# Kernel tuning notes

Measured on AMD Instinct MI355X. Metric: run time of the kernel, lower is better.

Reference implementation:

```python
import jax, jax.numpy as jnp
import numpy as np

N_IN, N_OUT, N_HID, N_RES = 16, 2, 256, 256
B, L = 64, 2048
ALPHA_FAST, ALPHA_SLOW, SIGMA_NEU = 1.0, 0.1, 0.05


def _linear_params(k, n_out, n_in):
    # mimics torch nn.Linear default init: U(-1/sqrt(fan_in), 1/sqrt(fan_in))
    bound = 1.0 / np.sqrt(n_in)
    kw, kb = jax.random.split(k)
    W = jax.random.uniform(kw, (n_out, n_in), minval=-bound, maxval=bound, dtype=jnp.float32)
    b = jax.random.uniform(kb, (n_out,), minval=-bound, maxval=bound, dtype=jnp.float32)
    return W, b


def setup_inputs() -> dict:
    key = jax.random.key(0)
    ks = jax.random.split(key, 11)
    W_in, b_in = _linear_params(ks[0], N_HID, N_IN)
    W_hh, b_hh = _linear_params(ks[1], N_HID, N_HID)
    W_sf, b_sf = _linear_params(ks[2], N_HID, N_RES)
    W_fs, b_fs = _linear_params(ks[3], N_RES, N_HID)
    W_res, b_res = _linear_params(ks[4], N_RES, N_RES)
    W_out, b_out = _linear_params(ks[5], N_OUT, N_HID)
    W_pr, b_pr = _linear_params(ks[6], N_IN, N_RES)
    input_signal = jax.random.normal(ks[7], (B, L, N_IN), dtype=jnp.float32)
    hidden = jax.random.normal(ks[8], (B, N_HID), dtype=jnp.float32)
    reservoir = jax.random.normal(ks[9], (B, N_RES), dtype=jnp.float32)
    # neural noise: randn * sigma_neu * sqrt(alpha_fast), precomputed time-major [L,B,H]
    noise = jax.random.normal(ks[10], (L, B, N_HID), dtype=jnp.float32) * (SIGMA_NEU * np.sqrt(ALPHA_FAST))
    return dict(input_signal=input_signal, hidden=hidden, reservoir=reservoir, noise=noise,
                W_in=W_in, b_in=b_in, W_hh=W_hh, b_hh=b_hh, W_sf=W_sf, b_sf=b_sf,
                W_fs=W_fs, b_fs=b_fs, W_res=W_res, b_res=b_res,
                W_out=W_out, b_out=b_out, W_pr=W_pr, b_pr=b_pr, length=L)


def reference(input_signal, hidden, reservoir, noise,
              W_in, b_in, W_hh, b_hh, W_sf, b_sf, W_fs, b_fs,
              W_res, b_res, W_out, b_out, W_pr, b_pr, length):
    xs = jnp.transpose(input_signal, (1, 0, 2))  # [L, B, n_in], time-major like torch permute
    af = jnp.float32(ALPHA_FAST)
    asl = jnp.float32(ALPHA_SLOW)

    def step(carry, inp):
        h, r = carry
        x_t, nz = inp
        tmp_h = jax.nn.relu(x_t @ W_in.T + b_in + h @ W_hh.T + b_hh + r @ W_sf.T + b_sf)
        tmp_r = jax.nn.relu(h @ W_fs.T + b_fs + r @ W_res.T + b_res)
        h = (1.0 - af) * h + af * tmp_h + nz
        r = (1.0 - asl) * r + asl * tmp_r
        out = jnp.clip(h @ W_out.T + b_out, -2.0, 2.0)
        prior = jax.nn.sigmoid(r @ W_pr.T + b_pr)
        return (h, r), (h, out, prior)

    _, (hs, outs, priors) = jax.lax.scan(step, (hidden, reservoir), (xs, noise))
    # back to batch-major [B, L, .]
    return (jnp.transpose(hs, (1, 0, 2)),
            jnp.transpose(outs, (1, 0, 2)),
            jnp.transpose(priors, (1, 0, 2)))
```

## Files before the change

kernel.cpp:

```cpp
#include <hip/hip_runtime.h>
#include <stdint.h>
#include <stddef.h>

#define LT    2048
#define BATCH 64
#define NH    256
#define HS_ELEMS  (BATCH * LT * NH)
#define OUT_ELEMS (BATCH * LT * 2)

typedef __attribute__((ext_vector_type(8))) __bf16 bf16x8;
typedef __attribute__((ext_vector_type(4))) float  f32x4;
typedef __attribute__((ext_vector_type(2))) unsigned u32x2;
typedef __attribute__((ext_vector_type(8))) unsigned short u16x8;

static __device__ __forceinline__ unsigned pk2(float a, float b) {
  unsigned r;
  asm("v_cvt_pk_bf16_f32 %0, %1, %2" : "=v"(r) : "v"(a), "v"(b));
  return r;
}
static __device__ __forceinline__ bf16x8 pack8v(f32x4 a, f32x4 b) {
  union { unsigned u[4]; bf16x8 v; } r;
  r.u[0] = pk2(a[0], a[1]); r.u[1] = pk2(a[2], a[3]);
  r.u[2] = pk2(b[0], b[1]); r.u[3] = pk2(b[2], b[3]);
  return r.v;
}
static __device__ __forceinline__ bf16x8 pack8(const float* p) {
  return pack8v(*(const f32x4*)p, *(const f32x4*)(p + 4));
}
static __device__ __forceinline__ float bf2f(unsigned short u) {
  unsigned v = ((unsigned)u) << 16;
  return __builtin_bit_cast(float, v);
}

#define BARRIER() do {                                           \
    asm volatile("s_waitcnt lgkmcnt(0)" ::: "memory");           \
    __builtin_amdgcn_s_barrier();                                \
    asm volatile("" ::: "memory");                               \
  } while (0)

#define W_RES_OFF 0
#define A_S0_OFF  131072
#define A_S1_OFF  147456
#define LDS_BYTES 163840

__global__ __launch_bounds__(256) void u_precompute_kernel(
    const float* __restrict__ x,
    const float* __restrict__ W_in,
    const float* __restrict__ b_in,
    const float* __restrict__ b_hh,
    const float* __restrict__ b_sf,
    float* __restrict__ u)
{
  __shared__ float xs[64][16];
  const int tid = threadIdx.x;
  const int b  = blockIdx.x >> 5;
  const int tc = (blockIdx.x & 31) << 6;
  float w[16];
#pragma unroll
  for (int i = 0; i < 16; ++i) w[i] = W_in[tid * 16 + i];
  const float bias = b_in[tid] + b_hh[tid] + b_sf[tid];
  for (int r = tid; r < 64 * 16; r += 256)
    xs[r >> 4][r & 15] = x[((size_t)b * LT + tc + (r >> 4)) * 16 + (r & 15)];
  __syncthreads();
  for (int tt = 0; tt < 64; ++tt) {
    float s = bias;
#pragma unroll
    for (int i = 0; i < 16; ++i) s += xs[tt][i] * w[i];
    u[((size_t)b * LT + tc + tt) * NH + tid] = s;
  }
}

template<int PRIOR_MODE>
__global__ __launch_bounds__(512, 1) void rnn_seq_kernel(
    const float* __restrict__ hidden,
    const float* __restrict__ reservoir,
    const float* __restrict__ noise,
    const float* __restrict__ W_hh, const float* __restrict__ W_sf,
    const float* __restrict__ W_fs, const float* __restrict__ W_res,
    const float* __restrict__ b_fs, const float* __restrict__ b_res,
    const float* __restrict__ W_pr, const float* __restrict__ b_pr,
    float* __restrict__ hs,
    float* __restrict__ priors,
    unsigned short* __restrict__ rws)
{
  extern __shared__ char lds[];
  const int tid  = threadIdx.x;
  const int lane = tid & 63;
  const int wv   = tid >> 6;
  const int col  = lane & 15;
  const int kg   = lane >> 4;
  const int b0   = blockIdx.x * 16;

#pragma unroll 4
  for (int j = 0; j < 16; ++j) {
    const int c   = j * 512 + tid;
    const int kk8 = c >> 10, n = (c >> 2) & 255, kgs = c & 3;
    *(bf16x8*)(lds + W_RES_OFF + c * 16) =
        pack8(W_res + (size_t)n * NH + kk8 * 32 + kgs * 8);
  }
  {
    const int kk = tid >> 6, l16 = tid & 63;
    const int kgs = l16 >> 4, m = l16 & 15;
    *(bf16x8*)(lds + A_S0_OFF + tid * 16) =
        pack8(hidden + (size_t)(b0 + m) * NH + kk * 32 + kgs * 8);
    *(bf16x8*)(lds + A_S0_OFF + (tid + 512) * 16) =
        pack8(reservoir + (size_t)(b0 + m) * NH + kk * 32 + kgs * 8);
  }

  bf16x8 wHH[2][8], wSF[2][8], wFS[2][8];
  f32x4 biasrR[2];
#pragma unroll
  for (int tile = 0; tile < 2; ++tile) {
    const int n = wv * 32 + tile * 16 + col;
#pragma unroll
    for (int kk = 0; kk < 8; ++kk) {
      wHH[tile][kk] = pack8(W_hh + (size_t)n * NH + kk * 32 + kg * 8);
      wSF[tile][kk] = pack8(W_sf + (size_t)n * NH + kk * 32 + kg * 8);
      wFS[tile][kk] = pack8(W_fs + (size_t)n * NH + kk * 32 + kg * 8);
    }
    const int nb = wv * 32 + tile * 16 + kg * 4;
    f32x4 bf = *(const f32x4*)(b_fs + nb);
    f32x4 br = *(const f32x4*)(b_res + nb);
    biasrR[tile] = bf + br;
  }
  bf16x8 wPR[PRIOR_MODE ? 8 : 1];
  f32x4 bp4;
  if (PRIOR_MODE) {
#pragma unroll
    for (int kk8 = 0; kk8 < 8; ++kk8)
      wPR[kk8] = pack8(W_pr + (size_t)col * NH + kk8 * 32 + kg * 8);
    bp4 = *(const f32x4*)(b_pr + kg * 4);
  }

  const size_t hsRow = (size_t)(b0 + col) * (LT * NH);
  const size_t nzRow = (size_t)(b0 + col) * NH;
  f32x4 r_old[2], accH[2], accR[2], accP;
#pragma unroll
  for (int tile = 0; tile < 2; ++tile) {
    const int nb = wv * 32 + tile * 16 + kg * 4;
    r_old[tile] = *(const f32x4*)(reservoir + nzRow + nb);
    accH[tile]  = *(const f32x4*)(hs + hsRow + nb);
    accR[tile]  = biasrR[tile];
  }
  if (PRIOR_MODE) accP = bp4;

  BARRIER();

#pragma unroll 1
  for (int t = 0; t < LT; ++t) {
    const size_t tp1 = (t + 1 < LT) ? (size_t)(t + 1) : (size_t)(LT - 1);
    f32x4 pfU[2], nzc[2];
#pragma unroll
    for (int tile = 0; tile < 2; ++tile) {
      const int nb = wv * 32 + tile * 16 + kg * 4;
      pfU[tile] = *(const f32x4*)(hs + hsRow + tp1 * NH + nb);
      nzc[tile] = *(const f32x4*)(noise + (size_t)t * (BATCH * NH) + nzRow + nb);
    }

    const char* afp = lds + A_S0_OFF + (t & 1) * 16384 + lane * 16;
    const char* bwp = lds + W_RES_OFF + (wv * 32) * 64 + col * 64 + kg * 16;
#pragma unroll
    for (int kk = 0; kk < 16; ++kk) {
      const bf16x8 af = *(const bf16x8*)(afp + kk * 1024);
      if (kk < 8) {
#pragma unroll
        for (int tile = 0; tile < 2; ++tile)
          accH[tile] = __builtin_amdgcn_mfma_f32_16x16x32_bf16(wHH[tile][kk], af, accH[tile], 0, 0, 0);
#pragma unroll
        for (int tile = 0; tile < 2; ++tile)
          accR[tile] = __builtin_amdgcn_mfma_f32_16x16x32_bf16(wFS[tile][kk], af, accR[tile], 0, 0, 0);
      } else {
#pragma unroll
        for (int tile = 0; tile < 2; ++tile)
          accH[tile] = __builtin_amdgcn_mfma_f32_16x16x32_bf16(wSF[tile][kk - 8], af, accH[tile], 0, 0, 0);
#pragma unroll
        for (int tile = 0; tile < 2; ++tile) {
          const bf16x8 bw = *(const bf16x8*)(bwp + (kk - 8) * 16384 + tile * 1024);
          accR[tile] = __builtin_amdgcn_mfma_f32_16x16x32_bf16(bw, af, accR[tile], 0, 0, 0);
        }
        if (PRIOR_MODE && wv == 1) {
          accP = __builtin_amdgcn_mfma_f32_16x16x32_bf16(wPR[kk - 8], af, accP, 0, 0, 0);
        }
      }
    }

    float* hsT = hs + hsRow + (size_t)t * NH;
    unsigned short* wsT = rws + ((size_t)(b0 + col) * LT + (size_t)t) * NH;
    char* abase = lds + A_S0_OFF + ((t + 1) & 1) * 16384 +
                  wv * 1024 + col * 16 + (kg & 1) * 8;
#pragma unroll
    for (int tile = 0; tile < 2; ++tile) {
      const int nb = wv * 32 + tile * 16 + kg * 4;
      f32x4 hv, rv;
#pragma unroll
      for (int j = 0; j < 4; ++j) {
        hv[j] = fmaxf(accH[tile][j], 0.f) + nzc[tile][j];
        rv[j] = 0.9f * r_old[tile][j] + 0.1f * fmaxf(accR[tile][j], 0.f);
      }
      r_old[tile] = rv;
      *(f32x4*)(hsT + nb) = hv;
      u32x2 hp, rp;
      hp[0] = pk2(hv[0], hv[1]); hp[1] = pk2(hv[2], hv[3]);
      rp[0] = pk2(rv[0], rv[1]); rp[1] = pk2(rv[2], rv[3]);
      char* dst = abase + (2 * tile + (kg >> 1)) * 256;
      *(u32x2*)dst          = hp;
      *(u32x2*)(dst + 8192) = rp;
      if (!PRIOR_MODE)
        *(u32x2*)(wsT + nb) = rp;
    }
    if (PRIOR_MODE && wv == 1 && t > 0) {
      f32x4 pv;
#pragma unroll
      for (int j = 0; j < 4; ++j) pv[j] = 1.f / (1.f + __expf(-accP[j]));
      *(f32x4*)(priors + (size_t)(b0 + col) * (LT * 16) + (size_t)(t - 1) * 16 + kg * 4) = pv;
    }

#pragma unroll
    for (int tile = 0; tile < 2; ++tile) {
      accH[tile] = pfU[tile];
      accR[tile] = biasrR[tile];
    }
    if (PRIOR_MODE) accP = bp4;
    BARRIER();
  }

  if (PRIOR_MODE && wv == 1) {
    f32x4 aP = bp4;
    const char* afp2 = lds + A_S0_OFF + 8192 + lane * 16;
#pragma unroll
    for (int kk8 = 0; kk8 < 8; ++kk8) {
      const bf16x8 af = *(const bf16x8*)(afp2 + kk8 * 1024);
      aP = __builtin_amdgcn_mfma_f32_16x16x32_bf16(wPR[kk8], af, aP, 0, 0, 0);
    }
    f32x4 pv;
#pragma unroll
    for (int j = 0; j < 4; ++j) pv[j] = 1.f / (1.f + __expf(-aP[j]));
    *(f32x4*)(priors + (size_t)(b0 + col) * (LT * 16) + (size_t)(LT - 1) * 16 + kg * 4) = pv;
  }
}

__global__ __launch_bounds__(256) void prior_post_kernel(
    const unsigned short* __restrict__ rws,
    const float* __restrict__ W_pr,
    const float* __restrict__ b_pr,
    float* __restrict__ priors)
{
  __shared__ unsigned short rs[64 * 256];
  const int tid = threadIdx.x;
  const int b  = blockIdx.x >> 5;
  const int tc = (blockIdx.x & 31) << 6;
  const unsigned short* src = rws + ((size_t)b * LT + tc) * NH;
  for (int i = tid; i < 2048; i += 256)
    *(((u16x8*)rs) + i) = *(((const u16x8*)src) + i);
  __syncthreads();
  const int n = tid & 15, tg = tid >> 4;
  const float* wrow = W_pr + n * NH;
  const float bp = b_pr[n];
  float s0 = bp, s1 = bp, s2 = bp, s3 = bp;
  const unsigned short* r0 = rs + (tg * 4 + 0) * NH;
#pragma unroll 8
  for (int k8 = 0; k8 < 32; ++k8) {
    const f32x4 w0 = *(const f32x4*)(wrow + k8 * 8);
    const f32x4 w1 = *(const f32x4*)(wrow + k8 * 8 + 4);
    const u16x8 a = *(const u16x8*)(r0 + k8 * 8);
    const u16x8 bq = *(const u16x8*)(r0 + NH + k8 * 8);
    const u16x8 c = *(const u16x8*)(r0 + 2 * NH + k8 * 8);
    const u16x8 d = *(const u16x8*)(r0 + 3 * NH + k8 * 8);
#pragma unroll
    for (int j = 0; j < 4; ++j) {
      s0 += bf2f(a[j]) * w0[j] + bf2f(a[j + 4]) * w1[j];
      s1 += bf2f(bq[j]) * w0[j] + bf2f(bq[j + 4]) * w1[j];
      s2 += bf2f(c[j]) * w0[j] + bf2f(c[j + 4]) * w1[j];
      s3 += bf2f(d[j]) * w0[j] + bf2f(d[j + 4]) * w1[j];
    }
  }
  float* dst = priors + ((size_t)b * LT + tc + tg * 4) * 16 + n;
  dst[0]  = 1.f / (1.f + __expf(-s0));
  dst[16] = 1.f / (1.f + __expf(-s1));
  dst[32] = 1.f / (1.f + __expf(-s2));
  dst[48] = 1.f / (1.f + __expf(-s3));
}

__global__ __launch_bounds__(256) void out_project_kernel(
    const float* __restrict__ hs,
    const float* __restrict__ W_out,
    const float* __restrict__ b_out,
    float* __restrict__ outs)
{
  const int tid = threadIdx.x;
  const int lane = tid & 63;
  const int wv = tid >> 6;
  const int row0 = blockIdx.x * 64 + wv * 16;
  f32x4 w0 = *(const f32x4*)(W_out + lane * 4);
  f32x4 w1 = *(const f32x4*)(W_out + 256 + lane * 4);
  const float bo0 = b_out[0], bo1 = b_out[1];
  for (int i = 0; i < 16; ++i) {
    const f32x4 h = *(const f32x4*)(hs + (size_t)(row0 + i) * NH + lane * 4);
    float p0 = h[0]*w0[0] + h[1]*w0[1] + h[2]*w0[2] + h[3]*w0[3];
    float p1 = h[0]*w1[0] + h[1]*w1[1] + h[2]*w1[2] + h[3]*w1[3];
#pragma unroll
    for (int off = 32; off; off >>= 1) {
      p0 += __shfl_down(p0, off, 64);
      p1 += __shfl_down(p1, off, 64);
    }
    if (lane == 0) {
      const size_t o = (size_t)(row0 + i) * 2;
      outs[o]     = fminf(fmaxf(p0 + bo0, -2.f), 2.f);
      outs[o + 1] = fminf(fmaxf(p1 + bo1, -2.f), 2.f);
    }
  }
}

extern "C" void kernel_launch(void* const* d_in, const int* in_sizes, int n_in,
                              void* d_out, int out_size, void* d_ws, size_t ws_size,
                              hipStream_t stream) {
  const float* x         = (const float*)d_in[0];
  const float* hidden    = (const float*)d_in[1];
  const float* reservoir = (const float*)d_in[2];
  const float* noise     = (const float*)d_in[3];
  const float* W_in      = (const float*)d_in[4];
  const float* b_in      = (const float*)d_in[5];
  const float* W_hh      = (const float*)d_in[6];
  const float* b_hh      = (const float*)d_in[7];
  const float* W_sf      = (const float*)d_in[8];
  const float* b_sf      = (const float*)d_in[9];
  const float* W_fs      = (const float*)d_in[10];
  const float* b_fs      = (const float*)d_in[11];
  const float* W_res     = (const float*)d_in[12];
  const float* b_res     = (const float*)d_in[13];
  const float* W_out     = (const float*)d_in[14];
  const float* b_out     = (const float*)d_in[15];
  const float* W_pr      = (const float*)d_in[16];
  const float* b_pr      = (const float*)d_in[17];

  float* hs     = (float*)d_out;
  float* outs   = hs + HS_ELEMS;
  float* priors = outs + OUT_ELEMS;
  unsigned short* rws = (unsigned short*)d_ws;

  const size_t rws_bytes = (size_t)BATCH * LT * NH * sizeof(unsigned short);

  u_precompute_kernel<<<2048, 256, 0, stream>>>(x, W_in, b_in, b_hh, b_sf, hs);

  if (ws_size >= rws_bytes) {
    hipFuncSetAttribute((const void*)&rnn_seq_kernel<0>,
                        hipFuncAttributeMaxDynamicSharedMemorySize, LDS_BYTES);
    rnn_seq_kernel<0><<<4, 512, LDS_BYTES, stream>>>(
        hidden, reservoir, noise, W_hh, W_sf, W_fs, W_res,
        b_fs, b_res, W_pr, b_pr, hs, priors, rws);
    prior_post_kernel<<<2048, 256, 0, stream>>>(rws, W_pr, b_pr, priors);
  } else {
    hipFuncSetAttribute((const void*)&rnn_seq_kernel<1>,
                        hipFuncAttributeMaxDynamicSharedMemorySize, LDS_BYTES);
    rnn_seq_kernel<1><<<4, 512, LDS_BYTES, stream>>>(
        hidden, reservoir, noise, W_hh, W_sf, W_fs, W_res,
        b_fs, b_res, W_pr, b_pr, hs, priors, rws);
  }

  out_project_kernel<<<2048, 256, 0, stream>>>(hs, W_out, b_out, outs);
}
```

Baseline: 6.530 ms.

## Halve recurrent kernel to 4 waves with single-buffered LDS state and coalesced reservoir spill

The sequential RNN kernel now runs 256 threads (4 waves) per block instead of 512, so each wave handles 64 output columns (4 tiles) and keeps three times as many weight fragments in registers. The double-buffered activation area is replaced by a single buffer with an extra barrier between the MFMA reads and the state writeback, and the combined reservoir bias moves into LDS. The bf16 reservoir spill is written in a thread-contiguous layout that the prior post-kernel unscatters through LDS. Fewer waves per barrier should cut synchronisation cost on this latency-bound recurrence, but each wave does twice the serial MFMA work per step, register pressure grows sharply, and the PRIOR_MODE path still gates on wv==1 with the old column mapping, so that fallback may be inconsistent.

Measured after the change: 9.099 ms. 1.39x slower.

```diff
diff --git a/kernel.cpp b/kernel.cpp
--- a/kernel.cpp
+++ b/kernel.cpp
@@ -39,9 +39,9 @@
   } while (0)
 
 #define W_RES_OFF 0
-#define A_S0_OFF  131072
-#define A_S1_OFF  147456
-#define LDS_BYTES 163840
+#define A_S_OFF   131072
+#define BIASR_OFF 147456
+#define LDS_BYTES 148480
 
 __global__ __launch_bounds__(256) void u_precompute_kernel(
     const float* __restrict__ x,
@@ -71,7 +71,7 @@
 }
 
 template<int PRIOR_MODE>
-__global__ __launch_bounds__(512, 1) void rnn_seq_kernel(
+__global__ __launch_bounds__(256, 1) void rnn_seq_kernel(
     const float* __restrict__ hidden,
     const float* __restrict__ reservoir,
     const float* __restrict__ noise,
@@ -81,7 +81,7 @@
     const float* __restrict__ W_pr, const float* __restrict__ b_pr,
     float* __restrict__ hs,
     float* __restrict__ priors,
-    unsigned short* __restrict__ rws)
+    u32x2* __restrict__ rws8)
 {
   extern __shared__ char lds[];
   const int tid  = threadIdx.x;
@@ -92,36 +92,38 @@
   const int b0   = blockIdx.x * 16;
 
 #pragma unroll 4
-  for (int j = 0; j < 16; ++j) {
-    const int c   = j * 512 + tid;
+  for (int j = 0; j < 32; ++j) {
+    const int c   = j * 256 + tid;
     const int kk8 = c >> 10, n = (c >> 2) & 255, kgs = c & 3;
     *(bf16x8*)(lds + W_RES_OFF + c * 16) =
         pack8(W_res + (size_t)n * NH + kk8 * 32 + kgs * 8);
   }
-  {
-    const int kk = tid >> 6, l16 = tid & 63;
+#pragma unroll
+  for (int half = 0; half < 2; ++half) {
+    const int c = half * 256 + tid;
+    const int kk = c >> 6, l16 = c & 63;
     const int kgs = l16 >> 4, m = l16 & 15;
-    *(bf16x8*)(lds + A_S0_OFF + tid * 16) =
+    *(bf16x8*)(lds + A_S_OFF + c * 16) =
         pack8(hidden + (size_t)(b0 + m) * NH + kk * 32 + kgs * 8);
-    *(bf16x8*)(lds + A_S0_OFF + (tid + 512) * 16) =
+    *(bf16x8*)(lds + A_S_OFF + (c + 512) * 16) =
         pack8(reservoir + (size_t)(b0 + m) * NH + kk * 32 + kgs * 8);
   }
-
-  bf16x8 wHH[2][8], wSF[2][8], wFS[2][8];
-  f32x4 biasrR[2];
-#pragma unroll
-  for (int tile = 0; tile < 2; ++tile) {
-    const int n = wv * 32 + tile * 16 + col;
+  if (tid < 64) {
+    f32x4 v = *(const f32x4*)(b_fs + tid * 4);
+    f32x4 w = *(const f32x4*)(b_res + tid * 4);
+    *(f32x4*)(lds + BIASR_OFF + tid * 16) = v + w;
+  }
+
+  bf16x8 wHH[4][8], wSF[4][8], wFS[4][8];
+#pragma unroll
+  for (int tile = 0; tile < 4; ++tile) {
+    const int n = wv * 64 + tile * 16 + col;
 #pragma unroll
     for (int kk = 0; kk < 8; ++kk) {
       wHH[tile][kk] = pack8(W_hh + (size_t)n * NH + kk * 32 + kg * 8);
       wSF[tile][kk] = pack8(W_sf + (size_t)n * NH + kk * 32 + kg * 8);
       wFS[tile][kk] = pack8(W_fs + (size_t)n * NH + kk * 32 + kg * 8);
     }
-    const int nb = wv * 32 + tile * 16 + kg * 4;
-    f32x4 bf = *(const f32x4*)(b_fs + nb);
-    f32x4 br = *(const f32x4*)(b_res + nb);
-    biasrR[tile] = bf + br;
   }
   bf16x8 wPR[PRIOR_MODE ? 8 : 1];
   f32x4 bp4;
@@ -134,13 +136,13 @@
 
   const size_t hsRow = (size_t)(b0 + col) * (LT * NH);
   const size_t nzRow = (size_t)(b0 + col) * NH;
-  f32x4 r_old[2], accH[2], accR[2], accP;
-#pragma unroll
-  for (int tile = 0; tile < 2; ++tile) {
-    const int nb = wv * 32 + tile * 16 + kg * 4;
+  f32x4 r_old[4], accH[4], accR[4], accP;
+#pragma unroll
+  for (int tile = 0; tile < 4; ++tile) {
+    const int nb = wv * 64 + tile * 16 + kg * 4;
     r_old[tile] = *(const f32x4*)(reservoir + nzRow + nb);
     accH[tile]  = *(const f32x4*)(hs + hsRow + nb);
-    accR[tile]  = biasrR[tile];
+    accR[tile]  = *(const f32x4*)(lds + BIASR_OFF + nb * 4);
   }
   if (PRIOR_MODE) accP = bp4;
 
@@ -149,32 +151,32 @@
 #pragma unroll 1
   for (int t = 0; t < LT; ++t) {
     const size_t tp1 = (t + 1 < LT) ? (size_t)(t + 1) : (size_t)(LT - 1);
-    f32x4 pfU[2], nzc[2];
-#pragma unroll
-    for (int tile = 0; tile < 2; ++tile) {
-      const int nb = wv * 32 + tile * 16 + kg * 4;
+    f32x4 pfU[4], nzc[4];
+#pragma unroll
+    for (int tile = 0; tile < 4; ++tile) {
+      const int nb = wv * 64 + tile * 16 + kg * 4;
       pfU[tile] = *(const f32x4*)(hs + hsRow + tp1 * NH + nb);
       nzc[tile] = *(const f32x4*)(noise + (size_t)t * (BATCH * NH) + nzRow + nb);
     }
 
-    const char* afp = lds + A_S0_OFF + (t & 1) * 16384 + lane * 16;
-    const char* bwp = lds + W_RES_OFF + (wv * 32) * 64 + col * 64 + kg * 16;
+    const char* afp = lds + A_S_OFF + lane * 16;
+    const char* bwp = lds + W_RES_OFF + (wv * 64) * 64 + col * 64 + kg * 16;
 #pragma unroll
     for (int kk = 0; kk < 16; ++kk) {
       const bf16x8 af = *(const bf16x8*)(afp + kk * 1024);
       if (kk < 8) {
 #pragma unroll
-        for (int tile = 0; tile < 2; ++tile)
+        for (int tile = 0; tile < 4; ++tile)
           accH[tile] = __builtin_amdgcn_mfma_f32_16x16x32_bf16(wHH[tile][kk], af, accH[tile], 0, 0, 0);
 #pragma unroll
-        for (int tile = 0; tile < 2; ++tile)
+        for (int tile = 0; tile < 4; ++tile)
           accR[tile] = __builtin_amdgcn_mfma_f32_16x16x32_bf16(wFS[tile][kk], af, accR[tile], 0, 0, 0);
       } else {
 #pragma unroll
-        for (int tile = 0; tile < 2; ++tile)
+        for (int tile = 0; tile < 4; ++tile)
           accH[tile] = __builtin_amdgcn_mfma_f32_16x16x32_bf16(wSF[tile][kk - 8], af, accH[tile], 0, 0, 0);
 #pragma unroll
-        for (int tile = 0; tile < 2; ++tile) {
+        for (int tile = 0; tile < 4; ++tile) {
           const bf16x8 bw = *(const bf16x8*)(bwp + (kk - 8) * 16384 + tile * 1024);
           accR[tile] = __builtin_amdgcn_mfma_f32_16x16x32_bf16(bw, af, accR[tile], 0, 0, 0);
         }
@@ -183,14 +185,13 @@
         }
       }
     }
+    BARRIER();
 
     float* hsT = hs + hsRow + (size_t)t * NH;
-    unsigned short* wsT = rws + ((size_t)(b0 + col) * LT + (size_t)t) * NH;
-    char* abase = lds + A_S0_OFF + ((t + 1) & 1) * 16384 +
-                  wv * 1024 + col * 16 + (kg & 1) * 8;
-#pragma unroll
-    for (int tile = 0; tile < 2; ++tile) {
-      const int nb = wv * 32 + tile * 16 + kg * 4;
+    char* abase = lds + A_S_OFF + wv * 2048 + col * 16 + (kg & 1) * 8;
+#pragma unroll
+    for (int tile = 0; tile < 4; ++tile) {
+      const int nb = wv * 64 + tile * 16 + kg * 4;
       f32x4 hv, rv;
 #pragma unroll
       for (int j = 0; j < 4; ++j) {
@@ -202,11 +203,11 @@
       u32x2 hp, rp;
       hp[0] = pk2(hv[0], hv[1]); hp[1] = pk2(hv[2], hv[3]);
       rp[0] = pk2(rv[0], rv[1]); rp[1] = pk2(rv[2], rv[3]);
-      char* dst = abase + (2 * tile + (kg >> 1)) * 256;
+      char* dst = abase + (tile >> 1) * 1024 + ((tile & 1) * 2 + (kg >> 1)) * 256;
       *(u32x2*)dst          = hp;
       *(u32x2*)(dst + 8192) = rp;
       if (!PRIOR_MODE)
-        *(u32x2*)(wsT + nb) = rp;
+        rws8[((size_t)blockIdx.x * LT + t) * 1024 + tile * 256 + tid] = rp;
     }
     if (PRIOR_MODE && wv == 1 && t > 0) {
       f32x4 pv;
@@ -216,9 +217,10 @@
     }
 
 #pragma unroll
-    for (int tile = 0; tile < 2; ++tile) {
+    for (int tile = 0; tile < 4; ++tile) {
+      const int nb = wv * 64 + tile * 16 + kg * 4;
       accH[tile] = pfU[tile];
-      accR[tile] = biasrR[tile];
+      accR[tile] = *(const f32x4*)(lds + BIASR_OFF + nb * 4);
     }
     if (PRIOR_MODE) accP = bp4;
     BARRIER();
@@ -226,7 +228,7 @@
 
   if (PRIOR_MODE && wv == 1) {
     f32x4 aP = bp4;
-    const char* afp2 = lds + A_S0_OFF + 8192 + lane * 16;
+    const char* afp2 = lds + A_S_OFF + 8192 + lane * 16;
 #pragma unroll
     for (int kk8 = 0; kk8 < 8; ++kk8) {
       const bf16x8 af = *(const bf16x8*)(afp2 + kk8 * 1024);
@@ -240,45 +242,46 @@
 }
 
 __global__ __launch_bounds__(256) void prior_post_kernel(
-    const unsigned short* __restrict__ rws,
+    const u32x2* __restrict__ rws8,
     const float* __restrict__ W_pr,
     const float* __restrict__ b_pr,
     float* __restrict__ priors)
 {
-  __shared__ unsigned short rs[64 * 256];
+  __shared__ unsigned short rs[8 * 16 * 256];
   const int tid = threadIdx.x;
-  const int b  = blockIdx.x >> 5;
-  const int tc = (blockIdx.x & 31) << 6;
-  const unsigned short* src = rws + ((size_t)b * LT + tc) * NH;
-  for (int i = tid; i < 2048; i += 256)
-    *(((u16x8*)rs) + i) = *(((const u16x8*)src) + i);
+  const int wg = blockIdx.x >> 8;
+  const int t0 = (blockIdx.x & 255) * 8;
+#pragma unroll 4
+  for (int i = 0; i < 32; ++i) {
+    const int ci = i * 256 + tid;
+    const int tt = ci >> 10, c = ci & 1023;
+    const u32x2 v = rws8[((size_t)wg * LT + t0 + tt) * 1024 + c];
+    const int tile = c >> 8, t2 = c & 255;
+    const int wvv = t2 >> 6, kgg = (t2 >> 4) & 3, cl = t2 & 15;
+    const int n0 = wvv * 64 + tile * 16 + kgg * 4;
+    *(u32x2*)(rs + ((tt * 16 + cl) << 8) + n0) = v;
+  }
   __syncthreads();
-  const int n = tid & 15, tg = tid >> 4;
+  const int n = tid & 15, g = tid >> 4;
   const float* wrow = W_pr + n * NH;
   const float bp = b_pr[n];
-  float s0 = bp, s1 = bp, s2 = bp, s3 = bp;
-  const unsigned short* r0 = rs + (tg * 4 + 0) * NH;
+  for (int pp = 0; pp < 8; ++pp) {
+    const int p = g * 8 + pp;
+    const int tt = p >> 4, cl = p & 15;
+    const unsigned short* rr = rs + ((tt * 16 + cl) << 8);
+    float s = bp;
 #pragma unroll 8
-  for (int k8 = 0; k8 < 32; ++k8) {
-    const f32x4 w0 = *(const f32x4*)(wrow + k8 * 8);
-    const f32x4 w1 = *(const f32x4*)(wrow + k8 * 8 + 4);
-    const u16x8 a = *(const u16x8*)(r0 + k8 * 8);
-    const u16x8 bq = *(const u16x8*)(r0 + NH + k8 * 8);
-    const u16x8 c = *(const u16x8*)(r0 + 2 * NH + k8 * 8);
-    const u16x8 d = *(const u16x8*)(r0 + 3 * NH + k8 * 8);
-#pragma unroll
-    for (int j = 0; j < 4; ++j) {
-      s0 += bf2f(a[j]) * w0[j] + bf2f(a[j + 4]) * w1[j];
-      s1 += bf2f(bq[j]) * w0[j] + bf2f(bq[j + 4]) * w1[j];
-      s2 += bf2f(c[j]) * w0[j] + bf2f(c[j + 4]) * w1[j];
-      s3 += bf2f(d[j]) * w0[j] + bf2f(d[j + 4]) * w1[j];
-    }
-  }
-  float* dst = priors + ((size_t)b * LT + tc + tg * 4) * 16 + n;
-  dst[0]  = 1.f / (1.f + __expf(-s0));
-  dst[16] = 1.f / (1.f + __expf(-s1));
-  dst[32] = 1.f / (1.f + __expf(-s2));
-  dst[48] = 1.f / (1.f + __expf(-s3));
+    for (int k8 = 0; k8 < 32; ++k8) {
+      const f32x4 w0 = *(const f32x4*)(wrow + k8 * 8);
+      const f32x4 w1 = *(const f32x4*)(wrow + k8 * 8 + 4);
+      const u16x8 a = *(const u16x8*)(rr + k8 * 8);
+#pragma unroll
+      for (int j = 0; j < 4; ++j)
+        s += bf2f(a[j]) * w0[j] + bf2f(a[j + 4]) * w1[j];
+    }
+    priors[((size_t)(wg * 16 + cl) * LT + t0 + tt) * 16 + n] =
+        1.f / (1.f + __expf(-s));
+  }
 }
 
 __global__ __launch_bounds__(256) void out_project_kernel(
@@ -336,7 +339,7 @@
   float* hs     = (float*)d_out;
   float* outs   = hs + HS_ELEMS;
   float* priors = outs + OUT_ELEMS;
-  unsigned short* rws = (unsigned short*)d_ws;
+  u32x2* rws8   = (u32x2*)d_ws;
 
   const size_t rws_bytes = (size_t)BATCH * LT * NH * sizeof(unsigned short);
 
@@ -345,16 +348,16 @@
   if (ws_size >= rws_bytes) {
     hipFuncSetAttribute((const void*)&rnn_seq_kernel<0>,
                         hipFuncAttributeMaxDynamicSharedMemorySize, LDS_BYTES);
-    rnn_seq_kernel<0><<<4, 512, LDS_BYTES, stream>>>(
+    rnn_seq_kernel<0><<<4, 256, LDS_BYTES, stream>>>(
         hidden, reservoir, noise, W_hh, W_sf, W_fs, W_res,
-        b_fs, b_res, W_pr, b_pr, hs, priors, rws);
-    prior_post_kernel<<<2048, 256, 0, stream>>>(rws, W_pr, b_pr, priors);
+        b_fs, b_res, W_pr, b_pr, hs, priors, rws8);
+    prior_post_kernel<<<1024, 256, 0, stream>>>(rws8, W_pr, b_pr, priors);
   } else {
     hipFuncSetAttribute((const void*)&rnn_seq_kernel<1>,
                         hipFuncAttributeMaxDynamicSharedMemorySize, LDS_BYTES);
-    rnn_seq_kernel<1><<<4, 512, LDS_BYTES, stream>>>(
+    rnn_seq_kernel<1><<<4, 256, LDS_BYTES, stream>>>(
         hidden, reservoir, noise, W_hh, W_sf, W_fs, W_res,
-        b_fs, b_res, W_pr, b_pr, hs, priors, rws);
+        b_fs, b_res, W_pr, b_pr, hs, priors, rws8);
   }
 
   out_project_kernel<<<2048, 256, 0, stream>>>(hs, W_out, b_out, outs);
```
